# Optimization experiments

Hardware: AMD Instinct MI355X
Metric: run time of the kernel (lower is better)

The kernel has to match this reference:

```python
import jax, jax.numpy as jnp
import numpy as np

HEADS = 16
HEAD_DIM = 64

def setup_inputs() -> dict:
    key = jax.random.key(0)
    ks = jax.random.split(key, 5)
    S, B, H = 1024, 4, 1024
    scale = 1.0 / np.sqrt(H)
    return {
        "hidden_states": jax.random.normal(ks[0], (S, B, H), jnp.float32),
        "attention_mask": jnp.zeros((B * HEADS, 1, S), jnp.float32),
        "Wq": jax.random.normal(ks[1], (H, H), jnp.float32) * scale,
        "bq": jnp.zeros((H,), jnp.float32),
        "Wk": jax.random.normal(ks[2], (H, H), jnp.float32) * scale,
        "bk": jnp.zeros((H,), jnp.float32),
        "Wv": jax.random.normal(ks[3], (H, H), jnp.float32) * scale,
        "bv": jnp.zeros((H,), jnp.float32),
    }

def reference(hidden_states, attention_mask, Wq, bq, Wk, bk, Wv, bv):
    S, B, H = hidden_states.shape
    d = HEAD_DIM
    inv_sqrt_d = 1.0 / np.sqrt(d)
    # QKV projections (torch Linear: x @ W.T + b)
    q = hidden_states @ Wq.T + bq  # (S, B, H)
    k = hidden_states @ Wk.T + bk
    v = hidden_states @ Wv.T + bv
    # (S, B*heads, d) -> (B*heads, S, d)
    q = q.reshape(S, B * HEADS, d).transpose(1, 0, 2)
    k = k.reshape(S, B * HEADS, d).transpose(1, 0, 2)
    v = v.reshape(S, B * HEADS, d).transpose(1, 0, 2)
    # SDDMM: scaled scores + additive mask -> (B*heads, S, S)
    scores = jnp.einsum('nsd,ntd->nst', q, k) * inv_sqrt_d + attention_mask
    probs = jax.nn.softmax(scores, axis=-1)
    # AV bmm -> (B*heads, S, d); note: dropout in source is seeded but never applied
    ctx = jnp.einsum('nst,ntd->nsd', probs, v)
    # back to (S, B, hidden)
    ctx = ctx.transpose(1, 0, 2).reshape(S, B, H)
    return ctx
```

## Files before the change

### kernel.cpp

```cpp
#include <hip/hip_runtime.h>
#include <hip/hip_bf16.h>
#include <math.h>

#define S_LEN 1024
#define BATCH 4
#define HID 1024
#define NHEADS 16
#define DHEAD 64
#define NTOT 64
#define M_ROWS 4096

typedef unsigned short u16;
typedef unsigned int u32;
typedef __bf16 bf16x8 __attribute__((ext_vector_type(8)));
typedef float f32x4 __attribute__((ext_vector_type(4)));

__device__ __forceinline__ u16 f2bf(float x) {
    __hip_bfloat16 h = __float2bfloat16(x);
    return *(u16*)&h;
}

__device__ __forceinline__ void gll16(const u16* g, u16* l) {
    __builtin_amdgcn_global_load_lds(
        (const __attribute__((address_space(1))) u32*)g,
        (__attribute__((address_space(3))) u32*)l, 16, 0, 0);
}

__global__ __launch_bounds__(256) void cvt_x(
    const float* __restrict__ src, u16* __restrict__ dst)
{
    int idx = (blockIdx.x * 256 + threadIdx.x) * 4;
    float4 x = *(const float4*)(src + idx);
    *(ushort4*)(dst + idx) = make_ushort4(f2bf(x.x), f2bf(x.y), f2bf(x.z), f2bf(x.w));
}

__global__ __launch_bounds__(256) void cvt_w(
    const float* __restrict__ wq, const float* __restrict__ wk,
    const float* __restrict__ wv, u16* __restrict__ dst)
{
    const float* s = (blockIdx.y == 0) ? wq : (blockIdx.y == 1) ? wk : wv;
    size_t off = (size_t)blockIdx.y * HID * HID;
    int idx = (blockIdx.x * 256 + threadIdx.x) * 4;
    float4 x = *(const float4*)(s + idx);
    *(ushort4*)(dst + off + idx) =
        make_ushort4(f2bf(x.x), f2bf(x.y), f2bf(x.z), f2bf(x.w));
}

__global__ __launch_bounds__(256, 3) void qkv_mfma(
    const u16* __restrict__ Xb, const u16* __restrict__ Wb,
    const float* __restrict__ bq, const float* __restrict__ bk,
    const float* __restrict__ bv,
    u16* __restrict__ Qb, u16* __restrict__ Kb, u16* __restrict__ Vb)
{
    const int m0 = blockIdx.x * 128;
    const int n0 = blockIdx.y * 128;
    const int which = blockIdx.z;

    __shared__ __align__(16) u16 As[128 * 32];
    __shared__ __align__(16) u16 Bs[128 * 32];

    const int tid = threadIdx.x;
    const int lane = tid & 63;
    const int w = tid >> 6;
    const int wm = w & 1, wn = w >> 1;
    const int quad = lane >> 4;
    const int l15 = lane & 15;

    const u16* W = Wb + (size_t)which * HID * HID;

    f32x4 acc[4][4];
    #pragma unroll
    for (int i = 0; i < 4; ++i)
        #pragma unroll
        for (int j = 0; j < 4; ++j)
            #pragma unroll
            for (int r = 0; r < 4; ++r) acc[i][j][r] = 0.0f;

    const int lrow = lane >> 2, lchk = (lane & 3) * 8;

    for (int k0 = 0; k0 < HID; k0 += 32) {
        #pragma unroll
        for (int c = 0; c < 2; ++c) {
            const int seg = w * 2 + c;
            const int row = seg * 16 + lrow;
            gll16(Xb + (size_t)(m0 + row) * HID + k0 + lchk, As + seg * 512);
            gll16(W  + (size_t)(n0 + row) * HID + k0 + lchk, Bs + seg * 512);
        }
        __syncthreads();

        bf16x8 af[4], bf[4];
        #pragma unroll
        for (int i = 0; i < 4; ++i)
            af[i] = *(const bf16x8*)(As + (wm * 64 + i * 16 + l15) * 32 + quad * 8);
        #pragma unroll
        for (int j = 0; j < 4; ++j)
            bf[j] = *(const bf16x8*)(Bs + (wn * 64 + j * 16 + l15) * 32 + quad * 8);
        #pragma unroll
        for (int i = 0; i < 4; ++i)
            #pragma unroll
            for (int j = 0; j < 4; ++j)
                acc[i][j] = __builtin_amdgcn_mfma_f32_16x16x32_bf16(
                    af[i], bf[j], acc[i][j], 0, 0, 0);
        __syncthreads();
    }

    const float* bias = (which == 0) ? bq : (which == 1) ? bk : bv;
    u16* Out = (which == 0) ? Qb : (which == 1) ? Kb : Vb;
    #pragma unroll
    for (int j = 0; j < 4; ++j) {
        const int o = n0 + wn * 64 + j * 16 + l15;
        const float bias_v = bias[o];
        const int head = o >> 6, d = o & 63;
        #pragma unroll
        for (int i = 0; i < 4; ++i) {
            #pragma unroll
            for (int r = 0; r < 4; ++r) {
                const int m = m0 + wm * 64 + i * 16 + quad * 4 + r;
                const int s = m >> 2, b = m & 3;
                const int n = b * NHEADS + head;
                Out[((size_t)n * S_LEN + s) * DHEAD + d] = f2bf(acc[i][j][r] + bias_v);
            }
        }
    }
}

__global__ __launch_bounds__(256) void vt_kernel(
    const u16* __restrict__ Vb, u16* __restrict__ VT)
{
    const int n = blockIdx.y;
    const int s0 = blockIdx.x * 64;
    __shared__ __align__(16) u16 Ls[64 * 72];
    const int tid = threadIdx.x;
    const size_t nbase = (size_t)n * S_LEN * DHEAD;

    #pragma unroll
    for (int q = 0; q < 2; ++q) {
        const int c = tid + 256 * q;
        const int t = c >> 3, kc = c & 7;
        *(uint4*)(Ls + t * 72 + kc * 8) =
            *(const uint4*)(Vb + nbase + (size_t)(s0 + t) * 64 + kc * 8);
    }
    __syncthreads();
    #pragma unroll
    for (int q = 0; q < 2; ++q) {
        const int c = tid + 256 * q;
        const int d = c >> 3, sc8 = (c & 7) * 8;
        union { uint4 u; u16 s[8]; } tmp;
        #pragma unroll
        for (int e = 0; e < 8; ++e) tmp.s[e] = Ls[(sc8 + e) * 72 + d];
        *(uint4*)(VT + nbase + (size_t)d * S_LEN + s0 + sc8) = tmp.u;
    }
}

__global__ __launch_bounds__(256, 4) void attn_mfma(
    const u16* __restrict__ Qb, const u16* __restrict__ Kb,
    const u16* __restrict__ VT, const float* __restrict__ mask,
    float* __restrict__ out)
{
    const int n = blockIdx.y;
    const int s0 = blockIdx.x * 64;
    const int b = n >> 4, head = n & 15;

    __shared__ __align__(16) u16 Kh[64 * 72];
    __shared__ __align__(16) u16 Vs[64 * 72];
    __shared__ __align__(16) u16 Ps[64 * 72];

    const int tid = threadIdx.x;
    const int lane = tid & 63;
    const int w = tid >> 6;
    const int quad = lane >> 4;
    const int l15 = lane & 15;
    const size_t nbase = (size_t)n * S_LEN * DHEAD;

    bf16x8 qf[2];
    #pragma unroll
    for (int st = 0; st < 2; ++st)
        qf[st] = *(const bf16x8*)(Qb + nbase + (size_t)(s0 + w * 16 + l15) * 64 +
                                  st * 32 + quad * 8);

    f32x4 O[4];
    float l_part[4];
    #pragma unroll
    for (int r = 0; r < 4; ++r) {
        l_part[r] = 0.0f;
        #pragma unroll
        for (int jt = 0; jt < 4; ++jt) O[jt][r] = 0.0f;
    }

    const int crow = tid >> 3, cchk = (tid & 7) * 8;

    for (int t0 = 0; t0 < S_LEN; t0 += 64) {
        __syncthreads();
        #pragma unroll
        for (int q = 0; q < 2; ++q) {
            const int row = crow + 32 * q;
            *(uint4*)(Kh + row * 72 + cchk) =
                *(const uint4*)(Kb + nbase + (size_t)(t0 + row) * 64 + cchk);
            *(uint4*)(Vs + row * 72 + cchk) =
                *(const uint4*)(VT + nbase + (size_t)row * S_LEN + t0 + cchk);
        }
        __syncthreads();

        f32x4 sc[4];
        #pragma unroll
        for (int j = 0; j < 4; ++j)
            #pragma unroll
            for (int r = 0; r < 4; ++r) sc[j][r] = 0.0f;
        #pragma unroll
        for (int st = 0; st < 2; ++st)
            #pragma unroll
            for (int j = 0; j < 4; ++j) {
                bf16x8 kf = *(const bf16x8*)(Kh + (j * 16 + l15) * 72 +
                                             st * 32 + quad * 8);
                sc[j] = __builtin_amdgcn_mfma_f32_16x16x32_bf16(qf[st], kf, sc[j], 0, 0, 0);
            }

        float mvm[4];
        #pragma unroll
        for (int j = 0; j < 4; ++j)
            mvm[j] = mask[(size_t)n * S_LEN + t0 + j * 16 + l15] - 16.0f;

        #pragma unroll
        for (int r = 0; r < 4; ++r) {
            const int prow = w * 16 + quad * 4 + r;
            #pragma unroll
            for (int j = 0; j < 4; ++j) {
                const float p = __expf(fmaf(sc[j][r], 0.125f, mvm[j]));
                l_part[r] += p;
                Ps[prow * 72 + j * 16 + l15] = f2bf(p);
            }
        }

        #pragma unroll
        for (int st = 0; st < 2; ++st) {
            bf16x8 pf = *(const bf16x8*)(Ps + (w * 16 + l15) * 72 + st * 32 + quad * 8);
            #pragma unroll
            for (int jt = 0; jt < 4; ++jt) {
                bf16x8 vf = *(const bf16x8*)(Vs + (jt * 16 + l15) * 72 +
                                             st * 32 + quad * 8);
                O[jt] = __builtin_amdgcn_mfma_f32_16x16x32_bf16(pf, vf, O[jt], 0, 0, 0);
            }
        }
    }

    #pragma unroll
    for (int r = 0; r < 4; ++r) {
        float lr = l_part[r];
        #pragma unroll
        for (int off = 8; off >= 1; off >>= 1) lr += __shfl_xor(lr, off);
        const float inv_l = 1.0f / lr;
        const int s = s0 + w * 16 + quad * 4 + r;
        #pragma unroll
        for (int jt = 0; jt < 4; ++jt) {
            const int d = jt * 16 + l15;
            out[(size_t)s * (BATCH * HID) + (size_t)b * HID + head * DHEAD + d] =
                O[jt][r] * inv_l;
        }
    }
}

extern "C" void kernel_launch(void* const* d_in, const int* in_sizes, int n_in,
                              void* d_out, int out_size, void* d_ws, size_t ws_size,
                              hipStream_t stream)
{
    const float* X    = (const float*)d_in[0];
    const float* mask = (const float*)d_in[1];
    const float* Wq   = (const float*)d_in[2];
    const float* bq   = (const float*)d_in[3];
    const float* Wk   = (const float*)d_in[4];
    const float* bk   = (const float*)d_in[5];
    const float* Wv   = (const float*)d_in[6];
    const float* bv   = (const float*)d_in[7];
    float* out = (float*)d_out;

    const size_t MX = (size_t)M_ROWS * HID;
    const size_t MW = (size_t)HID * HID;
    u16* wsp = (u16*)d_ws;
    u16* Xb = wsp;
    u16* Wb = Xb + MX;
    u16* Qb = Wb + 3 * MW;
    u16* Kb = Qb + MX;
    u16* Vb = Kb + MX;
    u16* VT = Vb + MX;

    cvt_x<<<dim3((int)(MX / 1024)), 256, 0, stream>>>(X, Xb);
    cvt_w<<<dim3((int)(MW / 1024), 3), 256, 0, stream>>>(Wq, Wk, Wv, Wb);
    qkv_mfma<<<dim3(M_ROWS / 128, HID / 128, 3), 256, 0, stream>>>(
        Xb, Wb, bq, bk, bv, Qb, Kb, Vb);
    vt_kernel<<<dim3(S_LEN / 64, NTOT), 256, 0, stream>>>(Vb, VT);
    attn_mfma<<<dim3(S_LEN / 64, NTOT), 256, 0, stream>>>(Qb, Kb, VT, mask, out);
}
```

Before: 163.8 us.

## Merge conversions, write V transposed in GEMM, double-buffer attention loads

Merges the two fp32-to-bf16 conversion kernels into one launch. The QKV GEMM epilogue now writes V straight into transposed layout, which removes the separate transpose kernel and its extra pass over memory. The attention kernel now handles 128 query rows per block and double-buffers K/V tiles through global_load_lds into XOR-swizzled LDS to overlap loads with MFMA and avoid bank conflicts. The conversion kernel also gains several redundant reloads, and the transposed V stores are strided, which may hurt GEMM epilogue efficiency.

```diff
diff --git a/kernel.cpp b/kernel.cpp
--- a/kernel.cpp
+++ b/kernel.cpp
@@ -26,31 +26,39 @@
         (__attribute__((address_space(3))) u32*)l, 16, 0, 0);
 }
 
-__global__ __launch_bounds__(256) void cvt_x(
-    const float* __restrict__ src, u16* __restrict__ dst)
+__global__ __launch_bounds__(256) void cvt_all(
+    const float* __restrict__ X, const float* __restrict__ wq,
+    const float* __restrict__ wk, const float* __restrict__ wv,
+    u16* __restrict__ Xb, u16* __restrict__ Wb)
 {
-    int idx = (blockIdx.x * 256 + threadIdx.x) * 4;
-    float4 x = *(const float4*)(src + idx);
-    *(ushort4*)(dst + idx) = make_ushort4(f2bf(x.x), f2bf(x.y), f2bf(x.z), f2bf(x.w));
-}
-
-__global__ __launch_bounds__(256) void cvt_w(
-    const float* __restrict__ wq, const float* __restrict__ wk,
-    const float* __restrict__ wv, u16* __restrict__ dst)
-{
-    const float* s = (blockIdx.y == 0) ? wq : (blockIdx.y == 1) ? wk : wv;
-    size_t off = (size_t)blockIdx.y * HID * HID;
-    int idx = (blockIdx.x * 256 + threadIdx.x) * 4;
-    float4 x = *(const float4*)(s + idx);
-    *(ushort4*)(dst + off + idx) =
-        make_ushort4(f2bf(x.x), f2bf(x.y), f2bf(x.z), f2bf(x.w));
+    const int bid = blockIdx.x;
+    const float* src;
+    u16* dst;
+    size_t base;
+    if (bid < 4096) {
+        src = X; dst = Xb; base = (size_t)bid * 1024;
+    } else {
+        const int wb = bid - 4096;
+        const int which = wb >> 10;
+        src = (which == 0) ? wq : (which == 1) ? wk : wv;
+        dst = Wb + (size_t)which * HID * HID;
+        base = (size_t)(wb & 1023) * 1024;
+    }
+    const size_t idx = base + threadIdx.x * 4;
+    float4 x = *(const float4*)(src + (bid < 4096 ? idx : (size_t)(idx - base) + base - ((bid < 4096) ? 0 : 0)));
+    x = *(const float4*)(src + ((bid < 4096) ? idx : (base - base) + idx - ((size_t)0)));
+    x = *(const float4*)(src + ((bid < 4096) ? idx : (idx - (size_t)0) - ((bid < 4096) ? 0 : (size_t)0)));
+    x = *(const float4*)(src + (bid < 4096 ? idx : idx - (size_t)0 - 0));
+    const size_t loc = (bid < 4096) ? idx : base + threadIdx.x * 4;
+    x = *(const float4*)(src + loc);
+    *(ushort4*)(dst + loc) = make_ushort4(f2bf(x.x), f2bf(x.y), f2bf(x.z), f2bf(x.w));
 }
 
 __global__ __launch_bounds__(256, 3) void qkv_mfma(
     const u16* __restrict__ Xb, const u16* __restrict__ Wb,
     const float* __restrict__ bq, const float* __restrict__ bk,
     const float* __restrict__ bv,
-    u16* __restrict__ Qb, u16* __restrict__ Kb, u16* __restrict__ Vb)
+    u16* __restrict__ Qb, u16* __restrict__ Kb, u16* __restrict__ VT)
 {
     const int m0 = blockIdx.x * 128;
     const int n0 = blockIdx.y * 128;
@@ -105,7 +113,6 @@
     }
 
     const float* bias = (which == 0) ? bq : (which == 1) ? bk : bv;
-    u16* Out = (which == 0) ? Qb : (which == 1) ? Kb : Vb;
     #pragma unroll
     for (int j = 0; j < 4; ++j) {
         const int o = n0 + wn * 64 + j * 16 + l15;
@@ -113,57 +120,35 @@
         const int head = o >> 6, d = o & 63;
         #pragma unroll
         for (int i = 0; i < 4; ++i) {
+            const int mbase = m0 + wm * 64 + i * 16 + quad * 4;
+            const int s = mbase >> 2;
             #pragma unroll
             for (int r = 0; r < 4; ++r) {
-                const int m = m0 + wm * 64 + i * 16 + quad * 4 + r;
-                const int s = m >> 2, b = m & 3;
-                const int n = b * NHEADS + head;
-                Out[((size_t)n * S_LEN + s) * DHEAD + d] = f2bf(acc[i][j][r] + bias_v);
-            }
-        }
-    }
-}
-
-__global__ __launch_bounds__(256) void vt_kernel(
-    const u16* __restrict__ Vb, u16* __restrict__ VT)
-{
-    const int n = blockIdx.y;
-    const int s0 = blockIdx.x * 64;
-    __shared__ __align__(16) u16 Ls[64 * 72];
-    const int tid = threadIdx.x;
-    const size_t nbase = (size_t)n * S_LEN * DHEAD;
-
-    #pragma unroll
-    for (int q = 0; q < 2; ++q) {
-        const int c = tid + 256 * q;
-        const int t = c >> 3, kc = c & 7;
-        *(uint4*)(Ls + t * 72 + kc * 8) =
-            *(const uint4*)(Vb + nbase + (size_t)(s0 + t) * 64 + kc * 8);
-    }
-    __syncthreads();
-    #pragma unroll
-    for (int q = 0; q < 2; ++q) {
-        const int c = tid + 256 * q;
-        const int d = c >> 3, sc8 = (c & 7) * 8;
-        union { uint4 u; u16 s[8]; } tmp;
-        #pragma unroll
-        for (int e = 0; e < 8; ++e) tmp.s[e] = Ls[(sc8 + e) * 72 + d];
-        *(uint4*)(VT + nbase + (size_t)d * S_LEN + s0 + sc8) = tmp.u;
-    }
-}
-
-__global__ __launch_bounds__(256, 4) void attn_mfma(
+                const int n = r * NHEADS + head;
+                const u16 hv = f2bf(acc[i][j][r] + bias_v);
+                if (which == 0)
+                    Qb[((size_t)n * S_LEN + s) * DHEAD + d] = hv;
+                else if (which == 1)
+                    Kb[((size_t)n * S_LEN + s) * DHEAD + d] = hv;
+                else
+                    VT[(size_t)n * (DHEAD * S_LEN) + (size_t)d * S_LEN + s] = hv;
+            }
+        }
+    }
+}
+
+__global__ __launch_bounds__(256, 2) void attn_mfma(
     const u16* __restrict__ Qb, const u16* __restrict__ Kb,
     const u16* __restrict__ VT, const float* __restrict__ mask,
     float* __restrict__ out)
 {
     const int n = blockIdx.y;
-    const int s0 = blockIdx.x * 64;
+    const int s0 = blockIdx.x * 128;
     const int b = n >> 4, head = n & 15;
 
-    __shared__ __align__(16) u16 Kh[64 * 72];
-    __shared__ __align__(16) u16 Vs[64 * 72];
-    __shared__ __align__(16) u16 Ps[64 * 72];
+    __shared__ __align__(16) u16 Kbuf[2][64 * 64];
+    __shared__ __align__(16) u16 Vbuf[2][64 * 64];
+    __shared__ __align__(16) u16 Ps[128 * 64];
 
     const int tid = threadIdx.x;
     const int lane = tid & 63;
@@ -172,48 +157,85 @@
     const int l15 = lane & 15;
     const size_t nbase = (size_t)n * S_LEN * DHEAD;
 
-    bf16x8 qf[2];
-    #pragma unroll
-    for (int st = 0; st < 2; ++st)
-        qf[st] = *(const bf16x8*)(Qb + nbase + (size_t)(s0 + w * 16 + l15) * 64 +
-                                  st * 32 + quad * 8);
-
-    f32x4 O[4];
-    float l_part[4];
-    #pragma unroll
-    for (int r = 0; r < 4; ++r) {
-        l_part[r] = 0.0f;
-        #pragma unroll
-        for (int jt = 0; jt < 4; ++jt) O[jt][r] = 0.0f;
-    }
-
-    const int crow = tid >> 3, cchk = (tid & 7) * 8;
-
-    for (int t0 = 0; t0 < S_LEN; t0 += 64) {
-        __syncthreads();
-        #pragma unroll
-        for (int q = 0; q < 2; ++q) {
-            const int row = crow + 32 * q;
-            *(uint4*)(Kh + row * 72 + cchk) =
-                *(const uint4*)(Kb + nbase + (size_t)(t0 + row) * 64 + cchk);
-            *(uint4*)(Vs + row * 72 + cchk) =
-                *(const uint4*)(VT + nbase + (size_t)row * S_LEN + t0 + cchk);
-        }
-        __syncthreads();
-
-        f32x4 sc[4];
-        #pragma unroll
-        for (int j = 0; j < 4; ++j)
-            #pragma unroll
-            for (int r = 0; r < 4; ++r) sc[j][r] = 0.0f;
+    int xs0 = ((quad ^ (l15 & 7)) * 8);
+    int xs1 = (((4 + quad) ^ (l15 & 7)) * 8);
+
+    const int srow = lane >> 3;
+    const int scg  = (lane & 7) ^ (srow & 7);
+
+    bf16x8 qf[2][2];
+    #pragma unroll
+    for (int mi = 0; mi < 2; ++mi)
         #pragma unroll
         for (int st = 0; st < 2; ++st)
-            #pragma unroll
-            for (int j = 0; j < 4; ++j) {
-                bf16x8 kf = *(const bf16x8*)(Kh + (j * 16 + l15) * 72 +
-                                             st * 32 + quad * 8);
-                sc[j] = __builtin_amdgcn_mfma_f32_16x16x32_bf16(qf[st], kf, sc[j], 0, 0, 0);
-            }
+            qf[mi][st] = *(const bf16x8*)(Qb + nbase +
+                (size_t)(s0 + w * 32 + mi * 16 + l15) * 64 + st * 32 + quad * 8);
+
+    f32x4 O[2][4];
+    float l_part[2][4];
+    #pragma unroll
+    for (int mi = 0; mi < 2; ++mi)
+        #pragma unroll
+        for (int r = 0; r < 4; ++r) {
+            l_part[mi][r] = 0.0f;
+            #pragma unroll
+            for (int jt = 0; jt < 4; ++jt) O[mi][jt][r] = 0.0f;
+        }
+
+    {
+        const u16* Kg = Kb + nbase;
+        const u16* Vg = VT + nbase;
+        #pragma unroll
+        for (int c = 0; c < 2; ++c) {
+            const int seg = w * 2 + c;
+            const int row = seg * 8 + srow;
+            gll16(Kg + (size_t)row * 64 + scg * 8, Kbuf[0] + seg * 512);
+            gll16(Vg + (size_t)row * S_LEN + scg * 8, Vbuf[0] + seg * 512);
+        }
+    }
+    __syncthreads();
+
+    for (int it = 0; it < 16; ++it) {
+        const int t0 = it * 64;
+        const u16* kb = Kbuf[it & 1];
+        const u16* vb = Vbuf[it & 1];
+
+        if (it < 15) {
+            const u16* Kg = Kb + nbase + (size_t)(t0 + 64) * 64;
+            const u16* Vg = VT + nbase + (t0 + 64);
+            u16* kd = Kbuf[(it + 1) & 1];
+            u16* vd = Vbuf[(it + 1) & 1];
+            #pragma unroll
+            for (int c = 0; c < 2; ++c) {
+                const int seg = w * 2 + c;
+                const int row = seg * 8 + srow;
+                gll16(Kg + (size_t)row * 64 + scg * 8, kd + seg * 512);
+                gll16(Vg + (size_t)row * S_LEN + scg * 8, vd + seg * 512);
+            }
+        }
+
+        f32x4 sc[2][4];
+        #pragma unroll
+        for (int mi = 0; mi < 2; ++mi)
+            #pragma unroll
+            for (int j = 0; j < 4; ++j)
+                #pragma unroll
+                for (int r = 0; r < 4; ++r) sc[mi][j][r] = 0.0f;
+
+        #pragma unroll
+        for (int st = 0; st < 2; ++st) {
+            const int xo = st ? xs1 : xs0;
+            bf16x8 kf[4];
+            #pragma unroll
+            for (int j = 0; j < 4; ++j)
+                kf[j] = *(const bf16x8*)(kb + (j * 16 + l15) * 64 + xo);
+            #pragma unroll
+            for (int mi = 0; mi < 2; ++mi)
+                #pragma unroll
+                for (int j = 0; j < 4; ++j)
+                    sc[mi][j] = __builtin_amdgcn_mfma_f32_16x16x32_bf16(
+                        qf[mi][st], kf[j], sc[mi][j], 0, 0, 0);
+        }
 
         float mvm[4];
         #pragma unroll
@@ -221,42 +243,56 @@
             mvm[j] = mask[(size_t)n * S_LEN + t0 + j * 16 + l15] - 16.0f;
 
         #pragma unroll
+        for (int mi = 0; mi < 2; ++mi)
+            #pragma unroll
+            for (int r = 0; r < 4; ++r) {
+                const int q = w * 32 + mi * 16 + quad * 4 + r;
+                const int q7 = (quad * 4 + r) & 7;
+                #pragma unroll
+                for (int j = 0; j < 4; ++j) {
+                    const float p = __expf(fmaf(sc[mi][j][r], 0.125f, mvm[j]));
+                    l_part[mi][r] += p;
+                    const int clog = j * 2 + (l15 >> 3);
+                    Ps[q * 64 + (clog ^ q7) * 8 + (l15 & 7)] = f2bf(p);
+                }
+            }
+
+        #pragma unroll
+        for (int st = 0; st < 2; ++st) {
+            const int xo = st ? xs1 : xs0;
+            bf16x8 vf[4];
+            #pragma unroll
+            for (int jt = 0; jt < 4; ++jt)
+                vf[jt] = *(const bf16x8*)(vb + (jt * 16 + l15) * 64 + xo);
+            #pragma unroll
+            for (int mi = 0; mi < 2; ++mi) {
+                bf16x8 pf = *(const bf16x8*)(Ps + (w * 32 + mi * 16 + l15) * 64 + xo);
+                #pragma unroll
+                for (int jt = 0; jt < 4; ++jt)
+                    O[mi][jt] = __builtin_amdgcn_mfma_f32_16x16x32_bf16(
+                        pf, vf[jt], O[mi][jt], 0, 0, 0);
+            }
+        }
+
+        __syncthreads();
+    }
+
+    #pragma unroll
+    for (int mi = 0; mi < 2; ++mi)
+        #pragma unroll
         for (int r = 0; r < 4; ++r) {
-            const int prow = w * 16 + quad * 4 + r;
-            #pragma unroll
-            for (int j = 0; j < 4; ++j) {
-                const float p = __expf(fmaf(sc[j][r], 0.125f, mvm[j]));
-                l_part[r] += p;
-                Ps[prow * 72 + j * 16 + l15] = f2bf(p);
-            }
-        }
-
-        #pragma unroll
-        for (int st = 0; st < 2; ++st) {
-            bf16x8 pf = *(const bf16x8*)(Ps + (w * 16 + l15) * 72 + st * 32 + quad * 8);
+            float lr = l_part[mi][r];
+            #pragma unroll
+            for (int off = 8; off >= 1; off >>= 1) lr += __shfl_xor(lr, off);
+            const float inv_l = 1.0f / lr;
+            const int s = s0 + w * 32 + mi * 16 + quad * 4 + r;
             #pragma unroll
             for (int jt = 0; jt < 4; ++jt) {
-                bf16x8 vf = *(const bf16x8*)(Vs + (jt * 16 + l15) * 72 +
-                                             st * 32 + quad * 8);
-                O[jt] = __builtin_amdgcn_mfma_f32_16x16x32_bf16(pf, vf, O[jt], 0, 0, 0);
-            }
-        }
-    }
-
-    #pragma unroll
-    for (int r = 0; r < 4; ++r) {
-        float lr = l_part[r];
-        #pragma unroll
-        for (int off = 8; off >= 1; off >>= 1) lr += __shfl_xor(lr, off);
-        const float inv_l = 1.0f / lr;
-        const int s = s0 + w * 16 + quad * 4 + r;
-        #pragma unroll
-        for (int jt = 0; jt < 4; ++jt) {
-            const int d = jt * 16 + l15;
-            out[(size_t)s * (BATCH * HID) + (size_t)b * HID + head * DHEAD + d] =
-                O[jt][r] * inv_l;
-        }
-    }
+                const int d = jt * 16 + l15;
+                out[(size_t)s * (BATCH * HID) + (size_t)b * HID + head * DHEAD + d] =
+                    O[mi][jt][r] * inv_l;
+            }
+        }
 }
 
 extern "C" void kernel_launch(void* const* d_in, const int* in_sizes, int n_in,
@@ -280,13 +316,10 @@
     u16* Wb = Xb + MX;
     u16* Qb = Wb + 3 * MW;
     u16* Kb = Qb + MX;
-    u16* Vb = Kb + MX;
-    u16* VT = Vb + MX;
-
-    cvt_x<<<dim3((int)(MX / 1024)), 256, 0, stream>>>(X, Xb);
-    cvt_w<<<dim3((int)(MW / 1024), 3), 256, 0, stream>>>(Wq, Wk, Wv, Wb);
+    u16* VT = Kb + MX;
+
+    cvt_all<<<dim3(4096 + 3072), 256, 0, stream>>>(X, Wq, Wk, Wv, Xb, Wb);
     qkv_mfma<<<dim3(M_ROWS / 128, HID / 128, 3), 256, 0, stream>>>(
-        Xb, Wb, bq, bk, bv, Qb, Kb, Vb);
-    vt_kernel<<<dim3(S_LEN / 64, NTOT), 256, 0, stream>>>(Vb, VT);
-    attn_mfma<<<dim3(S_LEN / 64, NTOT), 256, 0, stream>>>(Qb, Kb, VT, mask, out);
-}
+        Xb, Wb, bq, bk, bv, Qb, Kb, VT);
+    attn_mfma<<<dim3(S_LEN / 128, NTOT), 256, 0, stream>>>(Qb, Kb, VT, mask, out);
+}
```

Measured after the change: 166.0 us. No clear change (+1.4%).
